# Kernel optimization log

Measured on AMD Instinct MI355X. Metric: run time of the kernel, lower is better.

## Reference

```python
import jax, jax.numpy as jnp
import numpy as np

N = 10000      # nodes
E = 160000     # edges (avg degree 16)
R = 4          # num_relations
H = 3          # heads
B = 100        # graphs in the batch
ED = 8         # edge_dim
NEG = 0.2      # leaky_relu negative slope (PyG default)

CONVS = [(768, 128), (256, 384), (256, 128), (256, 128)]  # (in, out) per RGATConv
LINS = [(128, 256), (384, 256), (128, 256), (128, 256)]


def setup_inputs() -> dict:
    key = jax.random.key(0)
    ks = iter(jax.random.split(key, 64))
    p = lambda shape: jax.random.normal(next(ks), shape, dtype=jnp.float32) * 0.05
    inp = {
        "x": jax.random.normal(next(ks), (N, 768), dtype=jnp.float32),
        "edge_index": jax.random.randint(next(ks), (2, E), 0, N),
        "edge_type": jax.random.randint(next(ks), (E,), 0, R),
        "edge_attr": jax.random.normal(next(ks), (E, ED), dtype=jnp.float32),
        "batch": jnp.repeat(jnp.arange(B, dtype=jnp.int32), N // B),  # sorted graph ids
    }
    for i, (cin, cout) in enumerate(CONVS, 1):
        ho = H * cout
        inp[f"W{i}"] = p((R, cin, ho))
        inp[f"q{i}"] = p((ho, H))
        inp[f"k{i}"] = p((ho, H))
        inp[f"le{i}"] = p((ED, ho))
        inp[f"e{i}"] = p((ho, H))
        inp[f"b{i}"] = jnp.zeros((cout,), jnp.float32)
    for i, (cin, cout) in enumerate(LINS, 1):
        inp[f"lw{i}"] = p((cin, cout))
        inp[f"lb{i}"] = jnp.zeros((cout,), jnp.float32)
    return inp


def _segment_softmax(a, index, n):
    # softmax of per-edge scores a (E, H) over destination-node segments
    amax = jax.ops.segment_max(a, index, num_segments=n)
    amax = jnp.where(jnp.isfinite(amax), amax, 0.0)
    ex = jnp.exp(a - amax[index])
    s = jax.ops.segment_sum(ex, index, num_segments=n)
    return ex / jnp.maximum(s[index], 1e-16)


def _rgat(x, src, dst, etype, eattr, W, q, k, le, e, b, cout):
    n = x.shape[0]
    xW = jnp.einsum('ni,rio->nro', x, W)           # (N, R, H*O): per-relation transform
    qn = jnp.einsum('nro,oh->nrh', xW, q)          # node-level query scores
    kn = jnp.einsum('nro,oh->nrh', xW, k)          # node-level key scores
    qi = qn[dst, etype]                            # (E, H)
    kj = kn[src, etype]                            # (E, H)
    ae = (eattr @ le) @ e                          # (E, H) edge-feature scores
    alpha = jax.nn.leaky_relu(qi + kj + ae, NEG)
    alpha = _segment_softmax(alpha, dst, n)        # across-relation segment softmax
    outj = xW[src, etype].reshape(-1, H, cout)     # (E, H, O)
    msg = alpha[:, :, None] * outj
    aggr = jax.ops.segment_sum(msg, dst, num_segments=n)  # (N, H, O)
    return aggr.mean(axis=1) + b                   # concat=False -> mean over heads


def reference(x, edge_index, edge_type, edge_attr, batch,
              W1, q1, k1, le1, e1, b1, W2, q2, k2, le2, e2, b2,
              W3, q3, k3, le3, e3, b3, W4, q4, k4, le4, e4, b4,
              lw1, lb1, lw2, lb2, lw3, lb3, lw4, lb4):
    src, dst = edge_index[0], edge_index[1]
    convs = [(W1, q1, k1, le1, e1, b1), (W2, q2, k2, le2, e2, b2),
             (W3, q3, k3, le3, e3, b3), (W4, q4, k4, le4, e4, b4)]
    lins = [(lw1, lb1), (lw2, lb2), (lw3, lb3), (lw4, lb4)]
    h = x
    for (W, q, k, le, e, b), (lw, lb), (cin, cout) in zip(convs, lins, CONVS):
        h = _rgat(h, src, dst, edge_type, edge_attr, W, q, k, le, e, b, cout)
        h = h @ lw + lb
    # dropout is identity in eval; pick first node of each graph (hole node)
    hole_idx = jax.ops.segment_min(jnp.arange(h.shape[0]), batch, num_segments=B)
    return jax.nn.softmax(h[hole_idx], axis=1)     # (B, 256)
```

## Files before the change

kernel.cpp:

```cpp
#include <hip/hip_runtime.h>

typedef unsigned int uint;
typedef unsigned short ushort;
typedef __attribute__((ext_vector_type(8))) short bf16x8;
typedef __attribute__((ext_vector_type(4))) float f32x4;

#define GLD_LDS(g, l) __builtin_amdgcn_global_load_lds( \
    (const __attribute__((address_space(1))) void*)(g), \
    (__attribute__((address_space(3))) void*)(l), 16, 0, 0)

__device__ __forceinline__ ushort f2bf(float f) {
    uint u = __builtin_bit_cast(uint, f);
    u += 0x7fffu + ((u >> 16) & 1u);
    return (ushort)(u >> 16);
}
__device__ __forceinline__ float bf2f(ushort s) {
    uint u = ((uint)s) << 16;
    return __builtin_bit_cast(float, u);
}
__device__ __forceinline__ void wave_sync() {
    asm volatile("s_waitcnt lgkmcnt(0)" ::: "memory");
}
__device__ __forceinline__ float wave_max(float v) {
#pragma unroll
    for (int d = 32; d >= 1; d >>= 1) v = fmaxf(v, __shfl_xor(v, d));
    return v;
}
__device__ __forceinline__ float wave_sum(float v) {
#pragma unroll
    for (int d = 32; d >= 1; d >>= 1) v += __shfl_xor(v, d);
    return v;
}

__global__ void deg_hole_kernel(const int* __restrict__ dst, int* __restrict__ cnt,
                                const int* __restrict__ bat, int* __restrict__ hole,
                                int E, int N) {
    int e = blockIdx.x * 256 + threadIdx.x;
    if (e < E) atomicAdd(&cnt[dst[e]], 1);
    if (e < N) atomicMin(&hole[bat[e]], e);
}

__global__ void scan_kernel(const int* __restrict__ cnt, int* __restrict__ offs, int n) {
    __shared__ int part[1024];
    const int t = threadIdx.x;
    const int strip = (n + 1023) / 1024;
    int s = 0;
    for (int i = 0; i < strip; ++i) {
        int idx = t * strip + i;
        if (idx < n) s += cnt[idx];
    }
    part[t] = s;
    __syncthreads();
    for (int d = 1; d < 1024; d <<= 1) {
        int v = (t >= d) ? part[t - d] : 0;
        __syncthreads();
        part[t] += v;
        __syncthreads();
    }
    int run = (t == 0) ? 0 : part[t - 1];
    for (int i = 0; i < strip; ++i) {
        int idx = t * strip + i;
        if (idx < n) { offs[idx] = run; run += cnt[idx]; }
    }
    if (t == 1023) offs[n] = part[1023];
}

__global__ void fill_kernel(const int* __restrict__ dst, const int* __restrict__ offs,
                            int* __restrict__ cur, int* __restrict__ csr, int E) {
    int e = blockIdx.x * 256 + threadIdx.x;
    if (e < E) {
        int d = dst[e];
        int p = offs[d] + atomicAdd(&cur[d], 1);
        csr[p] = e;
    }
}

struct PrepWArgs {
    const float *x, *W0, *W2, *W3, *lw0, *lw1, *lw2, *lw3, *W1;
    ushort *hbf, *Wt0, *Wt2, *Wt3, *lwT0, *lwT1, *lwT2, *lwT3, *A2;
};

__device__ __forceinline__ void trW_body(const float* W, ushort* Wt, int cin, int ho, long idx) {
    long ncol = idx / cin;
    int c = (int)(idx % cin);
    int r = (int)(ncol / ho);
    int o = (int)(ncol % ho);
    Wt[idx] = f2bf(W[((long)r * cin + c) * ho + o]);
}
__device__ __forceinline__ void trLw_body(const float* lw, ushort* lwT, int cout_in, long idx) {
    int o = (int)(idx / cout_in);
    int c = (int)(idx % cout_in);
    lwT[idx] = f2bf(lw[(long)c * 256 + o]);
}

__global__ __launch_bounds__(256)
void prepw_kernel(PrepWArgs a, int nbCast, long nCast) {
    int b = blockIdx.x;
    const int t = threadIdx.x;
    if (b < nbCast) {
        long i = ((long)b * 256 + t) * 4;
        if (i + 4 <= nCast) {
            float4 v = *(const float4*)(a.x + i);
            ushort4 o4 = { f2bf(v.x), f2bf(v.y), f2bf(v.z), f2bf(v.w) };
            *(ushort4*)(a.hbf + i) = o4;
        }
        return;
    }
    b -= nbCast;
    if (b < 4608) { trW_body(a.W0, a.Wt0, 768, 384, (long)b * 256 + t); return; }
    b -= 4608;
    if (b < 1536) { trW_body(a.W2, a.Wt2, 256, 384, (long)b * 256 + t); return; }
    b -= 1536;
    if (b < 1536) { trW_body(a.W3, a.Wt3, 256, 384, (long)b * 256 + t); return; }
    b -= 1536;
    if (b < 128)  { trLw_body(a.lw0, a.lwT0, 128, (long)b * 256 + t); return; }
    b -= 128;
    if (b < 384)  { trLw_body(a.lw1, a.lwT1, 384, (long)b * 256 + t); return; }
    b -= 384;
    if (b < 128)  { trLw_body(a.lw2, a.lwT2, 128, (long)b * 256 + t); return; }
    b -= 128;
    if (b < 128)  { trLw_body(a.lw3, a.lwT3, 128, (long)b * 256 + t); return; }
    b -= 128;
    long idx = (long)b * 256 + t;
    int j = (int)(idx / 384), o = (int)(idx % 384);
    int h = j >> 10, rc = j & 1023;
    int r = rc >> 8, c = rc & 255;
    a.A2[idx] = f2bf(a.W1[((long)(r * 256 + c)) * 1152 + h * 384 + o] * (1.f / 3.f));
}

struct PrepSArgs {
    const float *W0, *W1, *W2, *W3, *q0, *q1, *q2, *q3, *k0, *k1, *k2, *k3;
    float *Wqk0, *Wqk1, *Wqk2, *Wqk3;
    const float *le0, *le1, *le2, *le3, *e0, *e1, *e2, *e3;
    float* g;
    const float *b2, *lw2l, *lb2;
    float* bf2;
};

__device__ __forceinline__ void wqk_body(const float* W, const float* q, const float* k,
                                         float* Wqk, int cin, int ho, int i, int lane) {
    int c = i / 24, j = i % 24;
    int r = j / 6, t6 = j % 6;
    const float* v = (t6 < 3) ? q : k;
    int h = t6 % 3;
    const float* wrow = W + ((long)r * cin + c) * ho;
    float s = 0.f;
    for (int o = lane; o < ho; o += 64) s += wrow[o] * v[(long)o * 3 + h];
    s = wave_sum(s);
    if (lane == 0) Wqk[i] = s;
}

__global__ __launch_bounds__(256)
void preps_kernel(PrepSArgs a) {
    const int wid = threadIdx.x >> 6, lane = threadIdx.x & 63;
    int w = blockIdx.x * 4 + wid;
    if (w < 96) {
        int l = w / 24, j = w % 24;
        int d = j / 3, h = j % 3;
        const float* le = (l == 0) ? a.le0 : (l == 1 ? a.le1 : (l == 2 ? a.le2 : a.le3));
        const float* e  = (l == 0) ? a.e0  : (l == 1 ? a.e1  : (l == 2 ? a.e2  : a.e3));
        int ho = (l == 1) ? 1152 : 384;
        float s = 0.f;
        for (int o = lane; o < ho; o += 64) s += le[(long)d * ho + o] * e[(long)o * 3 + h];
        s = wave_sum(s);
        if (lane == 0) a.g[l * 24 + j] = s;
        return;
    }
    w -= 96;
    if (w < 18432) { wqk_body(a.W0, a.q0, a.k0, a.Wqk0, 768, 384, w, lane); return; }
    w -= 18432;
    if (w < 6144)  { wqk_body(a.W1, a.q1, a.k1, a.Wqk1, 256, 1152, w, lane); return; }
    w -= 6144;
    if (w < 6144)  { wqk_body(a.W2, a.q2, a.k2, a.Wqk2, 256, 384, w, lane); return; }
    w -= 6144;
    if (w < 6144)  { wqk_body(a.W3, a.q3, a.k3, a.Wqk3, 256, 384, w, lane); return; }
    w -= 6144;
    if (w < 256) {
        float s = 0.f;
        for (int o = lane; o < 384; o += 64) s += a.b2[o] * a.lw2l[(long)o * 256 + w];
        s = wave_sum(s);
        if (lane == 0) a.bf2[w] = s + a.lb2[w];
    }
}

__global__ __launch_bounds__(256)
void prep2_kernel(const float* __restrict__ ea, const float* __restrict__ g,
                  float* __restrict__ aeb, int E, int nbAe,
                  const float* __restrict__ lw0, const float* __restrict__ Wqk1,
                  const float* __restrict__ lb0, ushort* __restrict__ lwT0, float* __restrict__ qb1,
                  const float* __restrict__ lw2, const float* __restrict__ Wqk3,
                  const float* __restrict__ lb2, ushort* __restrict__ lwT2, float* __restrict__ qb3) {
    int b = blockIdx.x;
    const int t = threadIdx.x;
    if (b < nbAe) {
        int e = b * 256 + t;
        if (e >= E) return;
        float a[8];
#pragma unroll
        for (int d = 0; d < 8; ++d) a[d] = ea[(long)e * 8 + d];
#pragma unroll
        for (int l = 0; l < 4; ++l) {
#pragma unroll
            for (int h = 0; h < 3; ++h) {
                float s = 0.f;
#pragma unroll
                for (int d = 0; d < 8; ++d) s += a[d] * g[l * 24 + d * 3 + h];
                aeb[((size_t)l * E + e) * 3 + h] = s;
            }
        }
        return;
    }
    b -= nbAe;
    const int wid = t >> 6, lane = t & 63;
    if (b < 768) {
        int w = b * 4 + wid;
        int c = w / 24, j = w % 24;
        float s = 0.f;
        for (int o = lane; o < 256; o += 64) s += lw0[(long)c * 256 + o] * Wqk1[(long)o * 24 + j];
        s = wave_sum(s);
        if (lane == 0) lwT0[(256 + j) * 128 + c] = f2bf(s);
        return;
    }
    b -= 768;
    if (b < 768) {
        int w = b * 4 + wid;
        int c = w / 24, j = w % 24;
        float s = 0.f;
        for (int o = lane; o < 256; o += 64) s += lw2[(long)c * 256 + o] * Wqk3[(long)o * 24 + j];
        s = wave_sum(s);
        if (lane == 0) lwT2[(256 + j) * 128 + c] = f2bf(s);
        return;
    }
    b -= 768;
    if (b < 6) {
        int w = b * 4 + wid;
        if (w < 24) {
            float s = 0.f;
            for (int o = lane; o < 256; o += 64) s += lb0[o] * Wqk1[(long)o * 24 + w];
            s = wave_sum(s);
            if (lane == 0) qb1[w] = s;
        }
        return;
    }
    b -= 6;
    if (b < 6) {
        int w = b * 4 + wid;
        if (w < 24) {
            float s = 0.f;
            for (int o = lane; o < 256; o += 64) s += lb2[o] * Wqk3[(long)o * 24 + w];
            s = wave_sum(s);
            if (lane == 0) qb3[w] = s;
        }
        return;
    }
    b -= 6;
    if (b < 52) { lwT0[280 * 128 + b * 256 + t] = 0; return; }
    b -= 52;
    lwT2[280 * 128 + b * 256 + t] = 0;
}

__global__ __launch_bounds__(256)
void qk_kernel(const float* __restrict__ h, const float* __restrict__ Wqk,
               float* __restrict__ qkn, int N, int cin) {
    const int wid = threadIdx.x >> 6, lane = threadIdx.x & 63;
    const int n = blockIdx.x * 4 + wid;
    if (n >= N) return;
    float acc[24];
#pragma unroll
    for (int j = 0; j < 24; ++j) acc[j] = 0.f;
    for (int c = lane; c < cin; c += 64) {
        float hv = h[(long)n * cin + c];
        const float* w = Wqk + (long)c * 24;
#pragma unroll
        for (int j = 0; j < 24; ++j) acc[j] += hv * w[j];
    }
#pragma unroll
    for (int j = 0; j < 24; ++j) {
        float v = wave_sum(acc[j]);
        if (lane == 0) qkn[(long)n * 24 + j] = v;
    }
}

template<int OUT_BF16, int DUAL, int PARTIAL, int QK>
__global__ __launch_bounds__(256, 5)
void gemm_bf16(const ushort* __restrict__ A, const ushort* __restrict__ Bt,
               void* __restrict__ Cp, ushort* __restrict__ C2,
               const float* __restrict__ bias,
               int M, int K, int ldc, int nbn, int nwg, int nbase, int Ks,
               float* __restrict__ qkn, const float* __restrict__ qb) {
    __shared__ ushort lA[2][128 * 32];
    __shared__ ushort lB[2][128 * 32];
    const int t = threadIdx.x;
    const int lane = t & 63;
    const int wid = t >> 6;

    int b = blockIdx.x;
    int q8 = nwg >> 3, r8 = nwg & 7;
    int xcd = b & 7, loc = b >> 3;
    int tt = (xcd < r8 ? xcd * (q8 + 1) : r8 * (q8 + 1) + (xcd - r8) * q8) + loc;
    const int slice = tt / nbase;
    const int tile = tt % nbase;
    const int kbase = slice * Ks;
    const int bm = (tile / nbn) * 128;
    const int bn = (tile % nbn) * 128;

    const int wr = (wid >> 1) * 64;
    const int wc = (wid & 1) * 64;

    f32x4 acc[4][4];
#pragma unroll
    for (int m = 0; m < 4; ++m)
#pragma unroll
        for (int nn = 0; nn < 4; ++nn) acc[m][nn] = (f32x4){0.f, 0.f, 0.f, 0.f};

    const int sr = t >> 2;
    const int sk = (((t & 3) ^ ((t >> 3) & 3)) * 8);
    long ar0 = bm + sr;      if (ar0 > M - 1) ar0 = M - 1;
    long ar1 = bm + sr + 64; if (ar1 > M - 1) ar1 = M - 1;
    const ushort* gA0 = A + ar0 * K + sk + kbase;
    const ushort* gA1 = A + ar1 * K + sk + kbase;
    const ushort* gB0 = Bt + (long)(bn + sr) * K + sk + kbase;
    const ushort* gB1 = Bt + (long)(bn + sr + 64) * K + sk + kbase;

    const int frow = lane & 15;
    const int pc8 = (((lane >> 4) ^ ((lane >> 1) & 3)) * 8);

    GLD_LDS(gA0, &lA[0][t * 8]);
    GLD_LDS(gA1, &lA[0][t * 8 + 64 * 32]);
    GLD_LDS(gB0, &lB[0][t * 8]);
    GLD_LDS(gB1, &lB[0][t * 8 + 64 * 32]);
    __syncthreads();

    int cur = 0;
    for (int k0 = 0; k0 < Ks; k0 += 32) {
        if (k0 + 32 < Ks) {
            int nb = cur ^ 1, kn = k0 + 32;
            GLD_LDS(gA0 + kn, &lA[nb][t * 8]);
            GLD_LDS(gA1 + kn, &lA[nb][t * 8 + 64 * 32]);
            GLD_LDS(gB0 + kn, &lB[nb][t * 8]);
            GLD_LDS(gB1 + kn, &lB[nb][t * 8 + 64 * 32]);
        }
        bf16x8 af[4], bff[4];
#pragma unroll
        for (int m = 0; m < 4; ++m)
            af[m] = *(const bf16x8*)&lA[cur][(wr + m * 16 + frow) * 32 + pc8];
#pragma unroll
        for (int nn = 0; nn < 4; ++nn)
            bff[nn] = *(const bf16x8*)&lB[cur][(wc + nn * 16 + frow) * 32 + pc8];
#pragma unroll
        for (int m = 0; m < 4; ++m)
#pragma unroll
            for (int nn = 0; nn < 4; ++nn)
                acc[m][nn] = __builtin_amdgcn_mfma_f32_16x16x32_bf16(af[m], bff[nn], acc[m][nn], 0, 0, 0);
        __syncthreads();
        cur ^= 1;
    }

    const int crow = (lane >> 4) * 4;
    const int ccol = lane & 15;
#pragma unroll
    for (int m = 0; m < 4; ++m) {
#pragma unroll
        for (int nn = 0; nn < 4; ++nn) {
            int col = bn + wc + nn * 16 + ccol;
#pragma unroll
            for (int r = 0; r < 4; ++r) {
                int row = bm + wr + m * 16 + crow + r;
                if (row < M) {
                    float v = acc[m][nn][r];
                    if (QK && col >= 256) {
                        int qc = col - 256;
                        if (qc < 24) qkn[(long)row * 24 + qc] = v + qb[qc];
                    } else {
                        if (!PARTIAL && bias) v += bias[col];
                        if (PARTIAL) {
                            ((float*)Cp)[(size_t)slice * M * ldc + (long)row * ldc + col] = v;
                        } else {
                            if (OUT_BF16) ((ushort*)Cp)[(long)row * ldc + col] = f2bf(v);
                            else          ((float*)Cp)[(long)row * ldc + col] = v;
                            if (DUAL)     C2[(long)row * ldc + col] = f2bf(v);
                        }
                    }
                }
            }
        }
    }
}

__global__ __launch_bounds__(256)
void reduce3qk_kernel(const float* __restrict__ P, const float* __restrict__ bf2,
                      const float* __restrict__ Wqk2,
                      float* __restrict__ outf, ushort* __restrict__ outb,
                      float* __restrict__ qkn, int M) {
    const int wid = threadIdx.x >> 6, lane = threadIdx.x & 63;
    const int n = blockIdx.x * 4 + wid;
    if (n >= M) return;
    long off = (long)n * 256 + lane * 4;
    const long stride = (long)M * 256;
    float4 a = *(const float4*)(P + off);
    float4 b = *(const float4*)(P + stride + off);
    float4 c = *(const float4*)(P + 2 * stride + off);
    float4 bs = *(const float4*)(bf2 + lane * 4);
    float rr[4] = { a.x + b.x + c.x + bs.x, a.y + b.y + c.y + bs.y,
                    a.z + b.z + c.z + bs.z, a.w + b.w + c.w + bs.w };
    float4 r4 = { rr[0], rr[1], rr[2], rr[3] };
    *(float4*)(outf + off) = r4;
    ushort4 o4 = { f2bf(rr[0]), f2bf(rr[1]), f2bf(rr[2]), f2bf(rr[3]) };
    *(ushort4*)(outb + off) = o4;
    float acc[24];
#pragma unroll
    for (int j = 0; j < 24; ++j) acc[j] = 0.f;
#pragma unroll
    for (int i = 0; i < 4; ++i) {
        const float* wr = Wqk2 + (long)(lane * 4 + i) * 24;
        float hv = rr[i];
#pragma unroll
        for (int j = 0; j < 24; ++j) acc[j] += hv * wr[j];
    }
#pragma unroll
    for (int j = 0; j < 24; ++j) {
        float v = wave_sum(acc[j]);
        if (lane == 0) qkn[(long)n * 24 + j] = v;
    }
}

__global__ __launch_bounds__(256)
void attn_kernel(const float* __restrict__ qkn, const ushort* __restrict__ xW,
                 const float* __restrict__ ae, const int* __restrict__ offs,
                 const int* __restrict__ csr, const int* __restrict__ srcv,
                 const int* __restrict__ etv, const float* __restrict__ bias,
                 ushort* __restrict__ out, int N) {
    __shared__ float4 pk_sh[4][64];
    __shared__ float red[4][384];
    const int wid = threadIdx.x >> 6, lane = threadIdx.x & 63;
    const int n = blockIdx.x * 4 + wid;
    if (n >= N) return;
    const int e0 = offs[n];
    const int deg = offs[n + 1] - e0;
    const float* qd = qkn + (long)n * 24;

    float m0 = -1e30f, m1 = -1e30f, m2 = -1e30f;
    for (int base = 0; base < deg; base += 64) {
        int idx = base + lane;
        if (idx < deg) {
            int eid = csr[e0 + idx];
            int s_ = srcv[eid], t_ = etv[eid];
            const float* qs = qkn + (long)s_ * 24 + t_ * 6;
            const float* a3 = ae + (long)eid * 3;
            float v0 = qd[t_ * 6 + 0] + qs[3] + a3[0];
            float v1 = qd[t_ * 6 + 1] + qs[4] + a3[1];
            float v2 = qd[t_ * 6 + 2] + qs[5] + a3[2];
            v0 = v0 > 0.f ? v0 : 0.2f * v0;
            v1 = v1 > 0.f ? v1 : 0.2f * v1;
            v2 = v2 > 0.f ? v2 : 0.2f * v2;
            m0 = fmaxf(m0, v0); m1 = fmaxf(m1, v1); m2 = fmaxf(m2, v2);
        }
    }
    m0 = wave_max(m0); m1 = wave_max(m1); m2 = wave_max(m2);

    float acc[6] = {0.f, 0.f, 0.f, 0.f, 0.f, 0.f};
    float ps0 = 0.f, ps1 = 0.f, ps2 = 0.f;

    for (int base = 0; base < deg; base += 64) {
        int cnt2 = deg - base; if (cnt2 > 64) cnt2 = 64;
        if (lane < cnt2) {
            int eid = csr[e0 + base + lane];
            int s_ = srcv[eid], t_ = etv[eid];
            const float* qs = qkn + (long)s_ * 24 + t_ * 6;
            const float* a3 = ae + (long)eid * 3;
            float v0 = qd[t_ * 6 + 0] + qs[3] + a3[0];
            float v1 = qd[t_ * 6 + 1] + qs[4] + a3[1];
            float v2 = qd[t_ * 6 + 2] + qs[5] + a3[2];
            v0 = v0 > 0.f ? v0 : 0.2f * v0;
            v1 = v1 > 0.f ? v1 : 0.2f * v1;
            v2 = v2 > 0.f ? v2 : 0.2f * v2;
            float p0 = __expf(v0 - m0), p1 = __expf(v1 - m1), p2 = __expf(v2 - m2);
            pk_sh[wid][lane] = make_float4(p0, p1, p2, __int_as_float((s_ << 2) | t_));
            ps0 += p0; ps1 += p1; ps2 += p2;
        }
        wave_sync();
        float4 pk0 = {0,0,0,0}, pk1 = {0,0,0,0}, pk2 = {0,0,0,0}, pk3 = {0,0,0,0};
        uint a0 = 0, b0 = 0, c0 = 0, a1 = 0, b1 = 0, c1 = 0;
        uint a2 = 0, b2 = 0, c2 = 0, a3 = 0, b3 = 0, c3 = 0;
#define LDE(S, J) { pk##S = pk_sh[wid][J]; \
    const uint* xr = (const uint*)(xW + (long)__float_as_int(pk##S.w) * 384); \
    a##S = xr[lane]; b##S = xr[lane + 64]; c##S = xr[lane + 128]; }
#define ACCE(S) { \
    acc[0] += pk##S.x * bf2f((ushort)(a##S & 0xffffu)); \
    acc[1] += pk##S.x * bf2f((ushort)(a##S >> 16)); \
    acc[2] += pk##S.y * bf2f((ushort)(b##S & 0xffffu)); \
    acc[3] += pk##S.y * bf2f((ushort)(b##S >> 16)); \
    acc[4] += pk##S.z * bf2f((ushort)(c##S & 0xffffu)); \
    acc[5] += pk##S.z * bf2f((ushort)(c##S >> 16)); }
        if (0 < cnt2) LDE(0, 0);
        if (1 < cnt2) LDE(1, 1);
        if (2 < cnt2) LDE(2, 2);
        if (3 < cnt2) LDE(3, 3);
        for (int j = 0; j < cnt2; j += 4) {
            { ACCE(0); if (j + 4 < cnt2) LDE(0, j + 4); }
            if (j + 1 < cnt2) { ACCE(1); if (j + 5 < cnt2) LDE(1, j + 5); }
            if (j + 2 < cnt2) { ACCE(2); if (j + 6 < cnt2) LDE(2, j + 6); }
            if (j + 3 < cnt2) { ACCE(3); if (j + 7 < cnt2) LDE(3, j + 7); }
        }
#undef LDE
#undef ACCE
        wave_sync();
    }
    ps0 = wave_sum(ps0); ps1 = wave_sum(ps1); ps2 = wave_sum(ps2);
    float i0 = 1.f / fmaxf(ps0, 1e-16f);
    float i1 = 1.f / fmaxf(ps1, 1e-16f);
    float i2 = 1.f / fmaxf(ps2, 1e-16f);
    red[wid][2 * lane]           = acc[0] * i0;
    red[wid][2 * lane + 1]       = acc[1] * i0;
    red[wid][128 + 2 * lane]     = acc[2] * i1;
    red[wid][128 + 2 * lane + 1] = acc[3] * i1;
    red[wid][256 + 2 * lane]     = acc[4] * i2;
    red[wid][256 + 2 * lane + 1] = acc[5] * i2;
    wave_sync();
    for (int o = lane; o < 128; o += 64) {
        float v = (red[wid][o] + red[wid][128 + o] + red[wid][256 + o]) * (1.f / 3.f) + bias[o];
        out[(long)n * 128 + o] = f2bf(v);
    }
}

__global__ __launch_bounds__(256)
void attn2_kernel(const float* __restrict__ qkn, const ushort* __restrict__ hbf,
                  const float* __restrict__ ae, const int* __restrict__ offs,
                  const int* __restrict__ csr, const int* __restrict__ srcv,
                  const int* __restrict__ etv, ushort* __restrict__ Z, int N) {
    __shared__ float4 pk_sh[4][64];
    const int wid = threadIdx.x >> 6, lane = threadIdx.x & 63;
    const int n = blockIdx.x * 4 + wid;
    if (n >= N) return;
    const int e0 = offs[n];
    const int deg = offs[n + 1] - e0;
    const float* qd = qkn + (long)n * 24;

    float m0 = -1e30f, m1 = -1e30f, m2 = -1e30f;
    for (int base = 0; base < deg; base += 64) {
        int idx = base + lane;
        if (idx < deg) {
            int eid = csr[e0 + idx];
            int s_ = srcv[eid], t_ = etv[eid];
            const float* qs = qkn + (long)s_ * 24 + t_ * 6;
            const float* a3 = ae + (long)eid * 3;
            float v0 = qd[t_ * 6 + 0] + qs[3] + a3[0];
            float v1 = qd[t_ * 6 + 1] + qs[4] + a3[1];
            float v2 = qd[t_ * 6 + 2] + qs[5] + a3[2];
            v0 = v0 > 0.f ? v0 : 0.2f * v0;
            v1 = v1 > 0.f ? v1 : 0.2f * v1;
            v2 = v2 > 0.f ? v2 : 0.2f * v2;
            m0 = fmaxf(m0, v0); m1 = fmaxf(m1, v1); m2 = fmaxf(m2, v2);
        }
    }
    m0 = wave_max(m0); m1 = wave_max(m1); m2 = wave_max(m2);

    float acc[48];
#pragma unroll
    for (int i = 0; i < 48; ++i) acc[i] = 0.f;
    float ps0 = 0.f, ps1 = 0.f, ps2 = 0.f;

    for (int base = 0; base < deg; base += 64) {
        int cnt2 = deg - base; if (cnt2 > 64) cnt2 = 64;
        if (lane < cnt2) {
            int eid = csr[e0 + base + lane];
            int s_ = srcv[eid], t_ = etv[eid];
            const float* qs = qkn + (long)s_ * 24 + t_ * 6;
            const float* a3 = ae + (long)eid * 3;
            float v0 = qd[t_ * 6 + 0] + qs[3] + a3[0];
            float v1 = qd[t_ * 6 + 1] + qs[4] + a3[1];
            float v2 = qd[t_ * 6 + 2] + qs[5] + a3[2];
            v0 = v0 > 0.f ? v0 : 0.2f * v0;
            v1 = v1 > 0.f ? v1 : 0.2f * v1;
            v2 = v2 > 0.f ? v2 : 0.2f * v2;
            float p0 = __expf(v0 - m0), p1 = __expf(v1 - m1), p2 = __expf(v2 - m2);
            pk_sh[wid][lane] = make_float4(p0, p1, p2, __int_as_float((s_ << 2) | t_));
            ps0 += p0; ps1 += p1; ps2 += p2;
        }
        wave_sync();
        float4 pk0 = {0,0,0,0}, pk1 = {0,0,0,0}, pk2 = {0,0,0,0}, pk3 = {0,0,0,0};
        uint2 v0_ = {0,0}, v1_ = {0,0}, v2_ = {0,0}, v3_ = {0,0};
#define LDE2(S, J) { pk##S = pk_sh[wid][J]; \
    v##S##_ = *(const uint2*)(hbf + ((long)(__float_as_int(pk##S.w) >> 2)) * 256 + lane * 4); }
#define UPDR(R) { \
    acc[(R)*4+0] += px * x0; acc[(R)*4+1] += px * x1; acc[(R)*4+2] += px * x2; acc[(R)*4+3] += px * x3; \
    acc[16+(R)*4+0] += py * x0; acc[16+(R)*4+1] += py * x1; acc[16+(R)*4+2] += py * x2; acc[16+(R)*4+3] += py * x3; \
    acc[32+(R)*4+0] += pz * x0; acc[32+(R)*4+1] += pz * x1; acc[32+(R)*4+2] += pz * x2; acc[32+(R)*4+3] += pz * x3; }
#define ACC2(S) { int r_ = __float_as_int(pk##S.w) & 3; \
    float x0 = bf2f((ushort)(v##S##_.x & 0xffffu)), x1 = bf2f((ushort)(v##S##_.x >> 16)); \
    float x2 = bf2f((ushort)(v##S##_.y & 0xffffu)), x3 = bf2f((ushort)(v##S##_.y >> 16)); \
    float px = pk##S.x, py = pk##S.y, pz = pk##S.z; \
    if (r_ == 0) UPDR(0) else if (r_ == 1) UPDR(1) else if (r_ == 2) UPDR(2) else UPDR(3) }
        if (0 < cnt2) LDE2(0, 0);
        if (1 < cnt2) LDE2(1, 1);
        if (2 < cnt2) LDE2(2, 2);
        if (3 < cnt2) LDE2(3, 3);
        for (int j = 0; j < cnt2; j += 4) {
            { ACC2(0); if (j + 4 < cnt2) LDE2(0, j + 4); }
            if (j + 1 < cnt2) { ACC2(1); if (j + 5 < cnt2) LDE2(1, j + 5); }
            if (j + 2 < cnt2) { ACC2(2); if (j + 6 < cnt2) LDE2(2, j + 6); }
            if (j + 3 < cnt2) { ACC2(3); if (j + 7 < cnt2) LDE2(3, j + 7); }
        }
#undef LDE2
#undef UPDR
#undef ACC2
        wave_sync();
    }
    ps0 = wave_sum(ps0); ps1 = wave_sum(ps1); ps2 = wave_sum(ps2);
    float inv0 = 1.f / fmaxf(ps0, 1e-16f);
    float inv1 = 1.f / fmaxf(ps1, 1e-16f);
    float inv2 = 1.f / fmaxf(ps2, 1e-16f);
    ushort* zr = Z + (long)n * 3072 + lane * 4;
#pragma unroll
    for (int h = 0; h < 3; ++h) {
        float iv = (h == 0) ? inv0 : (h == 1 ? inv1 : inv2);
#pragma unroll
        for (int r = 0; r < 4; ++r) {
            const float* a4 = acc + h * 16 + r * 4;
            ushort4 o4 = { f2bf(a4[0] * iv), f2bf(a4[1] * iv),
                           f2bf(a4[2] * iv), f2bf(a4[3] * iv) };
            *(ushort4*)(zr + h * 1024 + r * 256) = o4;
        }
    }
}

__global__ void softmax_kernel(const float* __restrict__ h, const int* __restrict__ hole,
                               float* __restrict__ out, int B) {
    int b = blockIdx.x;
    int t = threadIdx.x;
    int lane = t & 63, wid = t >> 6;
    __shared__ float sm[4];
    __shared__ float ss[4];
    int row = hole[b];
    float v = h[(long)row * 256 + t];
    float m = v;
#pragma unroll
    for (int d = 32; d >= 1; d >>= 1) m = fmaxf(m, __shfl_xor(m, d));
    if (lane == 0) sm[wid] = m;
    __syncthreads();
    m = fmaxf(fmaxf(sm[0], sm[1]), fmaxf(sm[2], sm[3]));
    float ex = __expf(v - m);
    float s = ex;
#pragma unroll
    for (int d = 32; d >= 1; d >>= 1) s += __shfl_xor(s, d);
    if (lane == 0) ss[wid] = s;
    __syncthreads();
    s = ss[0] + ss[1] + ss[2] + ss[3];
    out[(long)b * 256 + t] = ex / s;
}

extern "C" void kernel_launch(void* const* d_in, const int* in_sizes, int n_in,
                              void* d_out, int out_size, void* d_ws, size_t ws_size,
                              hipStream_t stream) {
    const float* x   = (const float*)d_in[0];
    const int*   ei  = (const int*)d_in[1];
    const int*   ety = (const int*)d_in[2];
    const float* ea  = (const float*)d_in[3];
    const int*   bat = (const int*)d_in[4];

    const int N = in_sizes[0] / 768;
    const int E = in_sizes[2];
    const int B = out_size / 256;

    static const int CIN[4]  = {768, 256, 256, 256};
    static const int COUT[4] = {128, 384, 128, 128};
    static const int NCC[4]  = {1536, 4608, 1536, 1536};

    const float *Wp[4], *qp[4], *kp[4], *lep[4], *ep[4], *bp[4], *lwp[4], *lbp[4];
    for (int l = 0; l < 4; ++l) {
        Wp[l]  = (const float*)d_in[5 + 6 * l];
        qp[l]  = (const float*)d_in[6 + 6 * l];
        kp[l]  = (const float*)d_in[7 + 6 * l];
        lep[l] = (const float*)d_in[8 + 6 * l];
        ep[l]  = (const float*)d_in[9 + 6 * l];
        bp[l]  = (const float*)d_in[10 + 6 * l];
        lwp[l] = (const float*)d_in[29 + 2 * l];
        lbp[l] = (const float*)d_in[30 + 2 * l];
    }

    char* ws = (char*)d_ws;
    size_t pos = 0;
    auto carve = [&](size_t bytes) -> char* {
        char* r = ws + pos;
        pos += (bytes + 255) & ~(size_t)255;
        return r;
    };
    ushort *Wt[4], *lwT[4];
    float* Wqk[4];
    for (int l = 0; l < 4; ++l) Wt[l]  = (ushort*)carve(l == 1 ? 0 : (size_t)2 * NCC[l] * CIN[l]);
    for (int l = 0; l < 4; ++l) lwT[l] = (ushort*)carve((size_t)2 * 384 * COUT[l]);
    for (int l = 0; l < 4; ++l) Wqk[l] = (float*)carve((size_t)4 * 24 * CIN[l]);
    float*  gbuf  = (float*)carve(4 * 24 * 4);
    float*  aeb   = (float*)carve((size_t)4 * E * 3 * 4);
    float*  qkn   = (float*)carve((size_t)N * 24 * 4);
    float*  qb1   = (float*)carve(24 * 4);
    float*  qb3   = (float*)carve(24 * 4);
    ushort* hbf   = (ushort*)carve((size_t)N * 768 * 2);
    ushort* xWb   = (ushort*)carve((size_t)N * 1536 * 2);
    ushort* Zb    = (ushort*)carve((size_t)N * 3072 * 2);
    ushort* A2    = (ushort*)carve((size_t)3072 * 384 * 2);
    ushort* W2T   = (ushort*)carve((size_t)256 * 3072 * 2);
    float*  bf2   = (float*)carve(256 * 4);
    ushort* convbf= (ushort*)carve((size_t)N * 384 * 2);
    float*  hbuf  = (float*)carve((size_t)N * 256 * 4);
    int* cnt  = (int*)carve((size_t)N * 4);
    int* cur  = (int*)carve((size_t)N * 4);
    int* offs = (int*)carve((size_t)(N + 1) * 4);
    int* csr  = (int*)carve((size_t)E * 4);
    int* hole = (int*)carve((size_t)B * 4);

    hipMemsetAsync(cnt, 0, (size_t)((char*)cur - (char*)cnt) + (size_t)N * 4, stream);
    hipMemsetAsync(hole, 0x7f, (size_t)B * 4, stream);

    const int* dst = ei + E;
    int nbEH = ((E > N ? E : N) + 255) / 256;
    deg_hole_kernel<<<nbEH, 256, 0, stream>>>(dst, cnt, bat, hole, E, N);
    scan_kernel<<<1, 1024, 0, stream>>>(cnt, offs, N);
    fill_kernel<<<(E + 255) / 256, 256, 0, stream>>>(dst, offs, cur, csr, E);

    long nCast = (long)N * 768;
    int nbCast = (int)((nCast / 4 + 255) / 256);
    PrepWArgs pw = { x, Wp[0], Wp[2], Wp[3], lwp[0], lwp[1], lwp[2], lwp[3], Wp[1],
                     hbf, Wt[0], Wt[2], Wt[3], lwT[0], lwT[1], lwT[2], lwT[3], A2 };
    prepw_kernel<<<nbCast + 13056, 256, 0, stream>>>(pw, nbCast, nCast);

    PrepSArgs ps = { Wp[0], Wp[1], Wp[2], Wp[3], qp[0], qp[1], qp[2], qp[3],
                     kp[0], kp[1], kp[2], kp[3], Wqk[0], Wqk[1], Wqk[2], Wqk[3],
                     lep[0], lep[1], lep[2], lep[3], ep[0], ep[1], ep[2], ep[3],
                     gbuf, bp[1], lwp[1], lbp[1], bf2 };
    preps_kernel<<<(37216 + 3) / 4, 256, 0, stream>>>(ps);

    int nbAe = (E + 255) / 256;
    prep2_kernel<<<nbAe + 1652, 256, 0, stream>>>(ea, gbuf, aeb, E, nbAe,
                                                  lwp[0], Wqk[1], lbp[0], lwT[0], qb1,
                                                  lwp[2], Wqk[3], lbp[2], lwT[2], qb3);

    gemm_bf16<1, 0, 0, 0><<<48, 256, 0, stream>>>(lwT[1], A2, (void*)W2T, nullptr, nullptr,
                                                  256, 384, 3072, 24, 48, 48, 384, nullptr, nullptr);
    qk_kernel<<<(N + 3) / 4, 256, 0, stream>>>(x, Wqk[0], qkn, N, 768);

    const int nbm = (N + 127) / 128;
    for (int l = 0; l < 4; ++l) {
        if (l == 1) {
            attn2_kernel<<<(N + 3) / 4, 256, 0, stream>>>(qkn, hbf, aeb + (size_t)l * E * 3,
                                                          offs, csr, ei, ety, Zb, N);
            int nbase = nbm * 2, nwgS = nbase * 3;
            gemm_bf16<0, 0, 1, 0><<<nwgS, 256, 0, stream>>>(Zb, W2T, (void*)xWb, nullptr, nullptr,
                                                            N, 3072, 256, 2, nwgS, nbase, 1024,
                                                            nullptr, nullptr);
            reduce3qk_kernel<<<(N + 3) / 4, 256, 0, stream>>>((const float*)xWb, bf2, Wqk[2],
                                                              hbuf, hbf, qkn, N);
        } else {
            int nbn1 = NCC[l] / 128, nwg1 = nbm * nbn1;
            gemm_bf16<1, 0, 0, 0><<<nwg1, 256, 0, stream>>>(hbf, Wt[l], (void*)xWb, nullptr, nullptr,
                                                            N, CIN[l], NCC[l], nbn1, nwg1, nwg1, CIN[l],
                                                            nullptr, nullptr);
            attn_kernel<<<(N + 3) / 4, 256, 0, stream>>>(qkn, xWb, aeb + (size_t)l * E * 3,
                                                         offs, csr, ei, ety, bp[l], convbf, N);
            if (l == 3) {
                int nwg2 = nbm * 2;
                gemm_bf16<0, 0, 0, 0><<<nwg2, 256, 0, stream>>>(convbf, lwT[3], (void*)hbuf, nullptr,
                                                                lbp[3], N, 128, 256, 2, nwg2, nwg2, 128,
                                                                nullptr, nullptr);
            } else {
                float* qbp = (l == 0) ? qb1 : qb3;
                int nwg2 = nbm * 3;
                gemm_bf16<0, 1, 0, 1><<<nwg2, 256, 0, stream>>>(convbf, lwT[l], (void*)hbuf, hbf,
                                                                lbp[l], N, 128, 256, 3, nwg2, nwg2, 128,
                                                                qkn, qbp);
            }
        }
    }
    softmax_kernel<<<B, 256, 0, stream>>>(hbuf, hole, (float*)d_out, B);
}
```

Measured before the change: 482.3 us.

## Fold layer-0 query/key projections into the first GEMM as extra columns

Removes the standalone fp32 qk_kernel for layer 0 by appending the 24 Wqk0 columns (zero-padded to a 128-wide tile) to the transposed bf16 weight Wt0. The layer-0 GEMM now runs 13 column tiles and writes those columns straight into qkn through a parameterised qkcol offset. The wqk precompute is also restructured so each wave computes all six q/k dot products for one (c, r) pair, which cuts the wave count. The cost is an extra padded output tile in the GEMM, bf16 precision on the layer-0 attention scores, and a new dependency ordering preps before prepw.

```diff
diff --git a/kernel.cpp b/kernel.cpp
--- a/kernel.cpp
+++ b/kernel.cpp
@@ -75,9 +75,75 @@
     }
 }
 
+struct PrepSArgs {
+    const float *W0, *W1, *W2, *W3, *q0, *q1, *q2, *q3, *k0, *k1, *k2, *k3;
+    float *Wqk0, *Wqk1, *Wqk2, *Wqk3;
+    const float *le0, *le1, *le2, *le3, *e0, *e1, *e2, *e3;
+    float* g;
+    const float *b2, *lw2l, *lb2;
+    float* bf2;
+};
+
+__device__ __forceinline__ void wqk_body(const float* W, const float* q, const float* k,
+                                         float* Wqk, int cin, int ho, int i, int lane) {
+    int c = i >> 2, r = i & 3;
+    const float* wrow = W + ((long)r * cin + c) * ho;
+    float sq0 = 0.f, sq1 = 0.f, sq2 = 0.f, sk0 = 0.f, sk1 = 0.f, sk2 = 0.f;
+    for (int o = lane; o < ho; o += 64) {
+        float w = wrow[o];
+        sq0 += w * q[(long)o * 3 + 0];
+        sq1 += w * q[(long)o * 3 + 1];
+        sq2 += w * q[(long)o * 3 + 2];
+        sk0 += w * k[(long)o * 3 + 0];
+        sk1 += w * k[(long)o * 3 + 1];
+        sk2 += w * k[(long)o * 3 + 2];
+    }
+    sq0 = wave_sum(sq0); sq1 = wave_sum(sq1); sq2 = wave_sum(sq2);
+    sk0 = wave_sum(sk0); sk1 = wave_sum(sk1); sk2 = wave_sum(sk2);
+    if (lane == 0) {
+        float* w6 = Wqk + (long)c * 24 + r * 6;
+        w6[0] = sq0; w6[1] = sq1; w6[2] = sq2;
+        w6[3] = sk0; w6[4] = sk1; w6[5] = sk2;
+    }
+}
+
+__global__ __launch_bounds__(256)
+void preps_kernel(PrepSArgs a) {
+    const int wid = threadIdx.x >> 6, lane = threadIdx.x & 63;
+    int w = blockIdx.x * 4 + wid;
+    if (w < 96) {
+        int l = w / 24, j = w % 24;
+        int d = j / 3, h = j % 3;
+        const float* le = (l == 0) ? a.le0 : (l == 1 ? a.le1 : (l == 2 ? a.le2 : a.le3));
+        const float* e  = (l == 0) ? a.e0  : (l == 1 ? a.e1  : (l == 2 ? a.e2  : a.e3));
+        int ho = (l == 1) ? 1152 : 384;
+        float s = 0.f;
+        for (int o = lane; o < ho; o += 64) s += le[(long)d * ho + o] * e[(long)o * 3 + h];
+        s = wave_sum(s);
+        if (lane == 0) a.g[l * 24 + j] = s;
+        return;
+    }
+    w -= 96;
+    if (w < 3072) { wqk_body(a.W0, a.q0, a.k0, a.Wqk0, 768, 384, w, lane); return; }
+    w -= 3072;
+    if (w < 1024) { wqk_body(a.W1, a.q1, a.k1, a.Wqk1, 256, 1152, w, lane); return; }
+    w -= 1024;
+    if (w < 1024) { wqk_body(a.W2, a.q2, a.k2, a.Wqk2, 256, 384, w, lane); return; }
+    w -= 1024;
+    if (w < 1024) { wqk_body(a.W3, a.q3, a.k3, a.Wqk3, 256, 384, w, lane); return; }
+    w -= 1024;
+    if (w < 256) {
+        float s = 0.f;
+        for (int o = lane; o < 384; o += 64) s += a.b2[o] * a.lw2l[(long)o * 256 + w];
+        s = wave_sum(s);
+        if (lane == 0) a.bf2[w] = s + a.lb2[w];
+    }
+}
+
 struct PrepWArgs {
     const float *x, *W0, *W2, *W3, *lw0, *lw1, *lw2, *lw3, *W1;
     ushort *hbf, *Wt0, *Wt2, *Wt3, *lwT0, *lwT1, *lwT2, *lwT3, *A2;
+    const float* Wqk0;
 };
 
 __device__ __forceinline__ void trW_body(const float* W, ushort* Wt, int cin, int ho, long idx) {
@@ -121,66 +187,23 @@
     b -= 128;
     if (b < 128)  { trLw_body(a.lw3, a.lwT3, 128, (long)b * 256 + t); return; }
     b -= 128;
-    long idx = (long)b * 256 + t;
-    int j = (int)(idx / 384), o = (int)(idx % 384);
-    int h = j >> 10, rc = j & 1023;
-    int r = rc >> 8, c = rc & 255;
-    a.A2[idx] = f2bf(a.W1[((long)(r * 256 + c)) * 1152 + h * 384 + o] * (1.f / 3.f));
-}
-
-struct PrepSArgs {
-    const float *W0, *W1, *W2, *W3, *q0, *q1, *q2, *q3, *k0, *k1, *k2, *k3;
-    float *Wqk0, *Wqk1, *Wqk2, *Wqk3;
-    const float *le0, *le1, *le2, *le3, *e0, *e1, *e2, *e3;
-    float* g;
-    const float *b2, *lw2l, *lb2;
-    float* bf2;
-};
-
-__device__ __forceinline__ void wqk_body(const float* W, const float* q, const float* k,
-                                         float* Wqk, int cin, int ho, int i, int lane) {
-    int c = i / 24, j = i % 24;
-    int r = j / 6, t6 = j % 6;
-    const float* v = (t6 < 3) ? q : k;
-    int h = t6 % 3;
-    const float* wrow = W + ((long)r * cin + c) * ho;
-    float s = 0.f;
-    for (int o = lane; o < ho; o += 64) s += wrow[o] * v[(long)o * 3 + h];
-    s = wave_sum(s);
-    if (lane == 0) Wqk[i] = s;
-}
-
-__global__ __launch_bounds__(256)
-void preps_kernel(PrepSArgs a) {
-    const int wid = threadIdx.x >> 6, lane = threadIdx.x & 63;
-    int w = blockIdx.x * 4 + wid;
-    if (w < 96) {
-        int l = w / 24, j = w % 24;
-        int d = j / 3, h = j % 3;
-        const float* le = (l == 0) ? a.le0 : (l == 1 ? a.le1 : (l == 2 ? a.le2 : a.le3));
-        const float* e  = (l == 0) ? a.e0  : (l == 1 ? a.e1  : (l == 2 ? a.e2  : a.e3));
-        int ho = (l == 1) ? 1152 : 384;
-        float s = 0.f;
-        for (int o = lane; o < ho; o += 64) s += le[(long)d * ho + o] * e[(long)o * 3 + h];
-        s = wave_sum(s);
-        if (lane == 0) a.g[l * 24 + j] = s;
-        return;
-    }
-    w -= 96;
-    if (w < 18432) { wqk_body(a.W0, a.q0, a.k0, a.Wqk0, 768, 384, w, lane); return; }
-    w -= 18432;
-    if (w < 6144)  { wqk_body(a.W1, a.q1, a.k1, a.Wqk1, 256, 1152, w, lane); return; }
-    w -= 6144;
-    if (w < 6144)  { wqk_body(a.W2, a.q2, a.k2, a.Wqk2, 256, 384, w, lane); return; }
-    w -= 6144;
-    if (w < 6144)  { wqk_body(a.W3, a.q3, a.k3, a.Wqk3, 256, 384, w, lane); return; }
-    w -= 6144;
-    if (w < 256) {
-        float s = 0.f;
-        for (int o = lane; o < 384; o += 64) s += a.b2[o] * a.lw2l[(long)o * 256 + w];
-        s = wave_sum(s);
-        if (lane == 0) a.bf2[w] = s + a.lb2[w];
-    }
+    if (b < 1728) {
+        long idx = (long)b * 256 + t;
+        int j = (int)(idx / 384), o = (int)(idx % 384);
+        int h = j >> 10, rc = j & 1023;
+        int r = rc >> 8, c = rc & 255;
+        a.A2[idx] = f2bf(a.W1[((long)(r * 256 + c)) * 1152 + h * 384 + o] * (1.f / 3.f));
+        return;
+    }
+    b -= 1728;
+    if (b < 72) {
+        long idx = (long)b * 256 + t;
+        int j = (int)(idx / 768), c = (int)(idx % 768);
+        a.Wt0[(long)(1536 + j) * 768 + c] = f2bf(a.Wqk0[(long)c * 24 + j]);
+        return;
+    }
+    b -= 72;
+    a.Wt0[(long)1560 * 768 + (long)b * 256 + t] = 0;
 }
 
 __global__ __launch_bounds__(256)
@@ -259,35 +282,13 @@
     lwT2[280 * 128 + b * 256 + t] = 0;
 }
 
-__global__ __launch_bounds__(256)
-void qk_kernel(const float* __restrict__ h, const float* __restrict__ Wqk,
-               float* __restrict__ qkn, int N, int cin) {
-    const int wid = threadIdx.x >> 6, lane = threadIdx.x & 63;
-    const int n = blockIdx.x * 4 + wid;
-    if (n >= N) return;
-    float acc[24];
-#pragma unroll
-    for (int j = 0; j < 24; ++j) acc[j] = 0.f;
-    for (int c = lane; c < cin; c += 64) {
-        float hv = h[(long)n * cin + c];
-        const float* w = Wqk + (long)c * 24;
-#pragma unroll
-        for (int j = 0; j < 24; ++j) acc[j] += hv * w[j];
-    }
-#pragma unroll
-    for (int j = 0; j < 24; ++j) {
-        float v = wave_sum(acc[j]);
-        if (lane == 0) qkn[(long)n * 24 + j] = v;
-    }
-}
-
 template<int OUT_BF16, int DUAL, int PARTIAL, int QK>
 __global__ __launch_bounds__(256, 5)
 void gemm_bf16(const ushort* __restrict__ A, const ushort* __restrict__ Bt,
                void* __restrict__ Cp, ushort* __restrict__ C2,
                const float* __restrict__ bias,
                int M, int K, int ldc, int nbn, int nwg, int nbase, int Ks,
-               float* __restrict__ qkn, const float* __restrict__ qb) {
+               float* __restrict__ qkn, const float* __restrict__ qb, int qkcol) {
     __shared__ ushort lA[2][128 * 32];
     __shared__ ushort lB[2][128 * 32];
     const int t = threadIdx.x;
@@ -368,9 +369,9 @@
                 int row = bm + wr + m * 16 + crow + r;
                 if (row < M) {
                     float v = acc[m][nn][r];
-                    if (QK && col >= 256) {
-                        int qc = col - 256;
-                        if (qc < 24) qkn[(long)row * 24 + qc] = v + qb[qc];
+                    if (QK && col >= qkcol) {
+                        int qc = col - qkcol;
+                        if (qc < 24) qkn[(long)row * 24 + qc] = v + (qb ? qb[qc] : 0.f);
                     } else {
                         if (!PARTIAL && bias) v += bias[col];
                         if (PARTIAL) {
@@ -687,7 +688,10 @@
     };
     ushort *Wt[4], *lwT[4];
     float* Wqk[4];
-    for (int l = 0; l < 4; ++l) Wt[l]  = (ushort*)carve(l == 1 ? 0 : (size_t)2 * NCC[l] * CIN[l]);
+    for (int l = 0; l < 4; ++l) {
+        size_t cols = (l == 0) ? 1664 : (size_t)NCC[l];
+        Wt[l] = (ushort*)carve(l == 1 ? 0 : (size_t)2 * cols * CIN[l]);
+    }
     for (int l = 0; l < 4; ++l) lwT[l] = (ushort*)carve((size_t)2 * 384 * COUT[l]);
     for (int l = 0; l < 4; ++l) Wqk[l] = (float*)carve((size_t)4 * 24 * CIN[l]);
     float*  gbuf  = (float*)carve(4 * 24 * 4);
@@ -718,17 +722,17 @@
     scan_kernel<<<1, 1024, 0, stream>>>(cnt, offs, N);
     fill_kernel<<<(E + 255) / 256, 256, 0, stream>>>(dst, offs, cur, csr, E);
 
+    PrepSArgs psa = { Wp[0], Wp[1], Wp[2], Wp[3], qp[0], qp[1], qp[2], qp[3],
+                      kp[0], kp[1], kp[2], kp[3], Wqk[0], Wqk[1], Wqk[2], Wqk[3],
+                      lep[0], lep[1], lep[2], lep[3], ep[0], ep[1], ep[2], ep[3],
+                      gbuf, bp[1], lwp[1], lbp[1], bf2 };
+    preps_kernel<<<(6496 + 3) / 4, 256, 0, stream>>>(psa);
+
     long nCast = (long)N * 768;
     int nbCast = (int)((nCast / 4 + 255) / 256);
     PrepWArgs pw = { x, Wp[0], Wp[2], Wp[3], lwp[0], lwp[1], lwp[2], lwp[3], Wp[1],
-                     hbf, Wt[0], Wt[2], Wt[3], lwT[0], lwT[1], lwT[2], lwT[3], A2 };
-    prepw_kernel<<<nbCast + 13056, 256, 0, stream>>>(pw, nbCast, nCast);
-
-    PrepSArgs ps = { Wp[0], Wp[1], Wp[2], Wp[3], qp[0], qp[1], qp[2], qp[3],
-                     kp[0], kp[1], kp[2], kp[3], Wqk[0], Wqk[1], Wqk[2], Wqk[3],
-                     lep[0], lep[1], lep[2], lep[3], ep[0], ep[1], ep[2], ep[3],
-                     gbuf, bp[1], lwp[1], lbp[1], bf2 };
-    preps_kernel<<<(37216 + 3) / 4, 256, 0, stream>>>(ps);
+                     hbf, Wt[0], Wt[2], Wt[3], lwT[0], lwT[1], lwT[2], lwT[3], A2, Wqk[0] };
+    prepw_kernel<<<nbCast + 13056 + 72 + 312, 256, 0, stream>>>(pw, nbCast, nCast);
 
     int nbAe = (E + 255) / 256;
     prep2_kernel<<<nbAe + 1652, 256, 0, stream>>>(ea, gbuf, aeb, E, nbAe,
@@ -736,8 +740,8 @@
                                                   lwp[2], Wqk[3], lbp[2], lwT[2], qb3);
 
     gemm_bf16<1, 0, 0, 0><<<48, 256, 0, stream>>>(lwT[1], A2, (void*)W2T, nullptr, nullptr,
-                                                  256, 384, 3072, 24, 48, 48, 384, nullptr, nullptr);
-    qk_kernel<<<(N + 3) / 4, 256, 0, stream>>>(x, Wqk[0], qkn, N, 768);
+                                                  256, 384, 3072, 24, 48, 48, 384,
+                                                  nullptr, nullptr, 0);
 
     const int nbm = (N + 127) / 128;
     for (int l = 0; l < 4; ++l) {
@@ -747,27 +751,35 @@
             int nbase = nbm * 2, nwgS = nbase * 3;
             gemm_bf16<0, 0, 1, 0><<<nwgS, 256, 0, stream>>>(Zb, W2T, (void*)xWb, nullptr, nullptr,
                                                             N, 3072, 256, 2, nwgS, nbase, 1024,
-                                                            nullptr, nullptr);
+                                                            nullptr, nullptr, 0);
             reduce3qk_kernel<<<(N + 3) / 4, 256, 0, stream>>>((const float*)xWb, bf2, Wqk[2],
                                                               hbuf, hbf, qkn, N);
         } else {
-            int nbn1 = NCC[l] / 128, nwg1 = nbm * nbn1;
-            gemm_bf16<1, 0, 0, 0><<<nwg1, 256, 0, stream>>>(hbf, Wt[l], (void*)xWb, nullptr, nullptr,
-                                                            N, CIN[l], NCC[l], nbn1, nwg1, nwg1, CIN[l],
-                                                            nullptr, nullptr);
+            if (l == 0) {
+                int nbn1 = 13, nwg1 = nbm * nbn1;
+                gemm_bf16<1, 0, 0, 1><<<nwg1, 256, 0, stream>>>(hbf, Wt[0], (void*)xWb, nullptr,
+                                                                nullptr, N, 768, 1536, nbn1, nwg1,
+                                                                nwg1, 768, qkn, nullptr, 1536);
+            } else {
+                int nbn1 = NCC[l] / 128, nwg1 = nbm * nbn1;
+                gemm_bf16<1, 0, 0, 0><<<nwg1, 256, 0, stream>>>(hbf, Wt[l], (void*)xWb, nullptr,
+                                                                nullptr, N, CIN[l], NCC[l], nbn1,
+                                                                nwg1, nwg1, CIN[l],
+                                                                nullptr, nullptr, 0);
+            }
             attn_kernel<<<(N + 3) / 4, 256, 0, stream>>>(qkn, xWb, aeb + (size_t)l * E * 3,
                                                          offs, csr, ei, ety, bp[l], convbf, N);
             if (l == 3) {
                 int nwg2 = nbm * 2;
                 gemm_bf16<0, 0, 0, 0><<<nwg2, 256, 0, stream>>>(convbf, lwT[3], (void*)hbuf, nullptr,
                                                                 lbp[3], N, 128, 256, 2, nwg2, nwg2, 128,
-                                                                nullptr, nullptr);
+                                                                nullptr, nullptr, 0);
             } else {
                 float* qbp = (l == 0) ? qb1 : qb3;
                 int nwg2 = nbm * 3;
                 gemm_bf16<0, 1, 0, 1><<<nwg2, 256, 0, stream>>>(convbf, lwT[l], (void*)hbuf, hbf,
                                                                 lbp[l], N, 128, 256, 3, nwg2, nwg2, 128,
-                                                                qkn, qbp);
+                                                                qkn, qbp, 256);
             }
         }
     }
```

After: 461.1 us. 4.4% less time.
